# Optimization experiments

Measured on AMD Instinct MI355X. Metric: run time of the kernel, lower is better.

## Reference

```python
import jax, jax.numpy as jnp
from jax import lax
import numpy as np

# Mamba mixer dims (mamba-1.4b scale)
D_MODEL, D_INNER, D_STATE, D_CONV, DT_RANK = 2048, 4096, 16, 4, 128
B, L = 2, 1024


def setup_inputs() -> dict:
    key = jax.random.key(0)
    ks = jax.random.split(key, 10)
    s = 0.02
    x = jax.random.normal(ks[0], (B, L, D_MODEL), jnp.float32)
    W_in = jax.random.normal(ks[1], (2 * D_INNER, D_MODEL), jnp.float32) * s
    conv_w = jax.random.normal(ks[2], (D_INNER, D_CONV), jnp.float32) * s  # depthwise kernel
    conv_b = jax.random.normal(ks[3], (D_INNER,), jnp.float32) * s
    W_x = jax.random.normal(ks[4], (DT_RANK + 2 * D_STATE, D_INNER), jnp.float32) * s
    W_dt = jax.random.normal(ks[5], (D_INNER, DT_RANK), jnp.float32) * s
    b_dt = jax.random.normal(ks[6], (D_INNER,), jnp.float32) * s
    # S4D-real init: A = -[1..d_state] per channel
    A_log = jnp.log(jnp.broadcast_to(jnp.arange(1, D_STATE + 1, dtype=jnp.float32), (D_INNER, D_STATE)))
    Dp = jnp.ones((D_INNER,), jnp.float32)
    W_out = jax.random.normal(ks[7], (D_MODEL, D_INNER), jnp.float32) * s
    return {"x": x, "W_in": W_in, "conv_w": conv_w, "conv_b": conv_b,
            "W_x": W_x, "W_dt": W_dt, "b_dt": b_dt, "A_log": A_log,
            "Dp": Dp, "W_out": W_out}


def reference(x, W_in, conv_w, conv_b, W_x, W_dt, b_dt, A_log, Dp, W_out):
    b, l, _ = x.shape
    d_inner, d_state = A_log.shape
    dt_rank = W_dt.shape[1]
    d_conv = conv_w.shape[1]

    # in_proj -> x branch and gate z   [b,l,2*d_inner]
    xz = jnp.einsum('bld,ed->ble', x, W_in)
    xp, z = jnp.split(xz, 2, axis=-1)

    # causal depthwise conv1d (kernel size d_conv) + SiLU
    xpad = jnp.pad(xp, ((0, 0), (d_conv - 1, 0), (0, 0)))
    xc = conv_b + sum(xpad[:, k:k + l, :] * conv_w[:, k] for k in range(d_conv))
    xc = jax.nn.silu(xc)

    # input-dependent dt, B, C
    dbc = jnp.einsum('ble,fe->blf', xc, W_x)
    dt = dbc[..., :dt_rank]
    Bm = dbc[..., dt_rank:dt_rank + d_state]          # [b,l,s]
    Cm = dbc[..., dt_rank + d_state:]                 # [b,l,s]
    delta = jax.nn.softplus(jnp.einsum('blr,er->ble', dt, W_dt) + b_dt)  # [b,l,e]

    A = -jnp.exp(A_log)                               # [e,s]
    dA = jnp.exp(delta[..., None] * A)                # [b,l,e,s]
    dBx = delta[..., None] * Bm[:, :, None, :] * xc[..., None]  # [b,l,e,s]

    def step(h, inp):
        dA_t, dBx_t = inp                             # [b,e,s]
        h = dA_t * h + dBx_t
        return h, h

    h0 = jnp.zeros((b, d_inner, d_state), x.dtype)
    _, hs = lax.scan(step, h0, (jnp.swapaxes(dA, 0, 1), jnp.swapaxes(dBx, 0, 1)))
    hs = jnp.swapaxes(hs, 0, 1)                       # [b,l,e,s]

    y = jnp.einsum('bles,bls->ble', hs, Cm) + xc * Dp
    y = y * jax.nn.silu(z)
    return jnp.einsum('ble,de->bld', y, W_out)
```

## Files before the change

### kernel.cpp

```cpp
#include <hip/hip_runtime.h>
#include <cstdint>


typedef __bf16 bf16x8 __attribute__((ext_vector_type(8)));
typedef float f32x4 __attribute__((ext_vector_type(4)));

__device__ __forceinline__ unsigned short f2bf(float f) {
  uint32_t u = __float_as_uint(f);
  u += 0x7FFFu + ((u >> 16) & 1u);
  return (unsigned short)(u >> 16);
}

__device__ __forceinline__ float silu_f(float v) {
  return v / (1.f + __expf(-v));
}

__device__ __forceinline__ float softplus_f(float v) {
  return (v > 20.f) ? v : log1pf(__expf(v));
}

__global__ void cast_f32_to_bf16(const float* __restrict__ src,
                                 unsigned short* __restrict__ dst, int n4) {
  int i = blockIdx.x * 256 + threadIdx.x;
  if (i >= n4) return;
  float4 v = reinterpret_cast<const float4*>(src)[i];
  ushort4 o;
  o.x = f2bf(v.x); o.y = f2bf(v.y); o.z = f2bf(v.z); o.w = f2bf(v.w);
  reinterpret_cast<ushort4*>(dst)[i] = o;
}

__global__ void cast_wx_pad(const float* __restrict__ Wx,
                            unsigned short* __restrict__ dst) {
  int i = blockIdx.x * 256 + threadIdx.x;
  int r = i >> 12;
  float v = (r < 160) ? Wx[(size_t)r * 4096 + (i & 4095)] : 0.f;
  dst[i] = f2bf(v);
}

#define BM 128
#define BN 128
#define BKK 32

__device__ __forceinline__ void stage_tile(const unsigned short* __restrict__ G,
                                           int ldK, int g0, int k0,
                                           unsigned short* lds, int wave, int lane) {
#pragma unroll
  for (int c = 0; c < 2; ++c) {
    int row = c * 64 + wave * 16 + (lane >> 2);
    int col = (lane & 3) * 8;
    const unsigned short* src = G + (size_t)(g0 + row) * ldK + (k0 + col);
    unsigned short* dst = lds + c * 2048 + wave * 512;
    __builtin_amdgcn_global_load_lds((__attribute__((address_space(1))) void*)(src),
                                     (__attribute__((address_space(3))) void*)(dst),
                                     16, 0, 0);
  }
}

__global__ __launch_bounds__(256)
void gemm_bt(const unsigned short* __restrict__ A, const unsigned short* __restrict__ B,
             float* __restrict__ C, int M, int N, int ldK, int kchunk,
             const float* __restrict__ bias_sp) {
  __shared__ unsigned short As[BM * BKK];
  __shared__ unsigned short Bs[BN * BKK];
  const int tid = threadIdx.x;
  const int wave = tid >> 6, lane = tid & 63;
  const int wr = wave >> 1, wc = wave & 1;
  const int m0 = blockIdx.y * BM, n0 = blockIdx.x * BN;
  const int lr = lane & 15, lg = lane >> 4;
  const int kb = blockIdx.z * kchunk, ke = kb + kchunk;
  C += (size_t)blockIdx.z * M * N;

  f32x4 zero = {0.f, 0.f, 0.f, 0.f};
  f32x4 acc[4][4];
#pragma unroll
  for (int i = 0; i < 4; ++i)
#pragma unroll
    for (int j = 0; j < 4; ++j) acc[i][j] = zero;

  for (int k0 = kb; k0 < ke; k0 += BKK) {
    stage_tile(A, ldK, m0, k0, As, wave, lane);
    stage_tile(B, ldK, n0, k0, Bs, wave, lane);
    __syncthreads();
    bf16x8 af[4], bfr[4];
#pragma unroll
    for (int i = 0; i < 4; ++i)
      af[i] = *reinterpret_cast<const bf16x8*>(&As[(wr * 64 + i * 16 + lr) * BKK + lg * 8]);
#pragma unroll
    for (int j = 0; j < 4; ++j)
      bfr[j] = *reinterpret_cast<const bf16x8*>(&Bs[(wc * 64 + j * 16 + lr) * BKK + lg * 8]);
#pragma unroll
    for (int i = 0; i < 4; ++i)
#pragma unroll
      for (int j = 0; j < 4; ++j)
        acc[i][j] = __builtin_amdgcn_mfma_f32_16x16x32_bf16(af[i], bfr[j], acc[i][j], 0, 0, 0);
    __syncthreads();
  }

#pragma unroll
  for (int i = 0; i < 4; ++i) {
#pragma unroll
    for (int j = 0; j < 4; ++j) {
      int mrow = m0 + wr * 64 + i * 16 + lg * 4;
      int ncol = n0 + wc * 64 + j * 16 + lr;
      if (bias_sp) {
        float bv = bias_sp[ncol];
#pragma unroll
        for (int r = 0; r < 4; ++r)
          C[(size_t)(mrow + r) * N + ncol] = softplus_f(acc[i][j][r] + bv);
      } else {
#pragma unroll
        for (int r = 0; r < 4; ++r)
          C[(size_t)(mrow + r) * N + ncol] = acc[i][j][r];
      }
    }
  }
}

__global__ void reduce8_dbc(const float* __restrict__ p, float* __restrict__ dbc,
                            unsigned short* __restrict__ dt_bf) {
  int i = blockIdx.x * 256 + threadIdx.x;
  float s = 0.f;
#pragma unroll
  for (int c = 0; c < 8; ++c) s += p[(size_t)c * 524288 + i];
  dbc[i] = s;
  int col = i & 255;
  if (col < 128) dt_bf[(size_t)(i >> 8) * 128 + col] = f2bf(s);
}

__global__ void reduce2_out(const float* __restrict__ p, float* __restrict__ out) {
  int i = blockIdx.x * 256 + threadIdx.x;
  const float4* p4 = reinterpret_cast<const float4*>(p);
  float4 a = p4[i], b = p4[i + 1048576];
  float4 r; r.x = a.x + b.x; r.y = a.y + b.y; r.z = a.z + b.z; r.w = a.w + b.w;
  reinterpret_cast<float4*>(out)[i] = r;
}

__global__ __launch_bounds__(512, 2)
void gemm_bt_8ph(const unsigned short* __restrict__ A,
                 const unsigned short* __restrict__ B,
                 float* __restrict__ C, int M, int N, int K, int nbm) {
  __shared__ unsigned short As[2][16384];
  __shared__ unsigned short Bs[2][16384];
  const int tid = threadIdx.x;
  const int wid = tid >> 6, lane = tid & 63;
  const int wr = wid >> 2, wc = wid & 3;
  const int lr = lane & 15, lg = lane >> 4;

  const int cpx = gridDim.x >> 3;
  const int x = blockIdx.x;
  const int wg = (x & 7) * cpx + (x >> 3);
  const int bm = wg % nbm, bn = wg / nbm;
  const int m0 = bm * 256, n0 = bn * 256;

  const int strow = tid >> 3;
  const int stcol0 = (tid & 7) * 8;

  f32x4 acc[8][4];
  f32x4 zero = {0.f, 0.f, 0.f, 0.f};
#pragma unroll
  for (int i = 0; i < 8; ++i)
#pragma unroll
    for (int j = 0; j < 4; ++j) acc[i][j] = zero;

  const int nt = K / 64;

  auto QUANT = [&](int t, int q) {
    const int buf = t & 1;
    const unsigned short* G = (q < 2) ? A : B;
    const int g0 = ((q < 2) ? m0 : n0) + ((q & 1) ? 128 : 0);
    unsigned short* lds = ((q < 2) ? &As[buf][0] : &Bs[buf][0]) + ((q & 1) ? 8192 : 0);
    const int k0 = t * 64;
#pragma unroll
    for (int r = 0; r < 2; ++r) {
      int row = r * 64 + strow;
      int scol = stcol0 ^ ((row & 7) << 3);
      const unsigned short* src = G + (size_t)(g0 + row) * K + (k0 + scol);
      __builtin_amdgcn_global_load_lds(
          (__attribute__((address_space(1))) const void*)(src),
          (__attribute__((address_space(3))) void*)(lds + r * 4096 + tid * 8),
          16, 0, 0);
    }
  };

  auto RD_A = [&](int buf, int mf, int ks) -> bf16x8 {
    int row = wr * 128 + mf * 16 + lr;
    int col = (ks * 32 + lg * 8) ^ ((row & 7) << 3);
    return *reinterpret_cast<const bf16x8*>(&As[buf][row * 64 + col]);
  };
  auto RD_B = [&](int buf, int nf, int ks) -> bf16x8 {
    int row = wc * 64 + nf * 16 + lr;
    int col = (ks * 32 + lg * 8) ^ ((row & 7) << 3);
    return *reinterpret_cast<const bf16x8*>(&Bs[buf][row * 64 + col]);
  };

  QUANT(0, 0); QUANT(0, 1); QUANT(0, 2); QUANT(0, 3);
  QUANT(1, 0);

  bf16x8 a[4][2], b[4][2];
  for (int t = 0; t < nt; ++t) {
    const int buf = t & 1;
    const bool pf1 = (t + 1 < nt);
    if (pf1) {
      QUANT(t + 1, 1);
      asm volatile("s_waitcnt vmcnt(4)" ::: "memory");
    } else {
      asm volatile("s_waitcnt vmcnt(0)" ::: "memory");
    }
    __builtin_amdgcn_s_barrier();
#pragma unroll
    for (int mf = 0; mf < 4; ++mf)
#pragma unroll
      for (int ks = 0; ks < 2; ++ks) a[mf][ks] = RD_A(buf, mf, ks);
#pragma unroll
    for (int nf = 0; nf < 2; ++nf)
#pragma unroll
      for (int ks = 0; ks < 2; ++ks) b[nf][ks] = RD_B(buf, nf, ks);
    asm volatile("s_waitcnt lgkmcnt(0)" ::: "memory");
    __builtin_amdgcn_sched_barrier(0);
    __builtin_amdgcn_s_setprio(1);
#pragma unroll
    for (int nf = 0; nf < 2; ++nf)
#pragma unroll
      for (int mf = 0; mf < 4; ++mf)
#pragma unroll
        for (int ks = 0; ks < 2; ++ks)
          acc[mf][nf] = __builtin_amdgcn_mfma_f32_16x16x32_bf16(a[mf][ks], b[nf][ks], acc[mf][nf], 0, 0, 0);
    __builtin_amdgcn_s_setprio(0);
    if (pf1) QUANT(t + 1, 2);
#pragma unroll
    for (int nf = 2; nf < 4; ++nf)
#pragma unroll
      for (int ks = 0; ks < 2; ++ks) b[nf][ks] = RD_B(buf, nf, ks);
    asm volatile("s_waitcnt lgkmcnt(0)" ::: "memory");
    __builtin_amdgcn_sched_barrier(0);
    __builtin_amdgcn_s_setprio(1);
#pragma unroll
    for (int nf = 2; nf < 4; ++nf)
#pragma unroll
      for (int mf = 0; mf < 4; ++mf)
#pragma unroll
        for (int ks = 0; ks < 2; ++ks)
          acc[mf][nf] = __builtin_amdgcn_mfma_f32_16x16x32_bf16(a[mf][ks], b[nf][ks], acc[mf][nf], 0, 0, 0);
    __builtin_amdgcn_s_setprio(0);
    if (pf1) QUANT(t + 1, 3);
#pragma unroll
    for (int mf = 0; mf < 4; ++mf)
#pragma unroll
      for (int ks = 0; ks < 2; ++ks) a[mf][ks] = RD_A(buf, mf + 4, ks);
    asm volatile("s_waitcnt lgkmcnt(0)" ::: "memory");
    __builtin_amdgcn_sched_barrier(0);
    __builtin_amdgcn_s_setprio(1);
#pragma unroll
    for (int nf = 0; nf < 2; ++nf)
#pragma unroll
      for (int mf = 0; mf < 4; ++mf)
#pragma unroll
        for (int ks = 0; ks < 2; ++ks)
          acc[mf + 4][nf] = __builtin_amdgcn_mfma_f32_16x16x32_bf16(a[mf][ks], b[nf][ks], acc[mf + 4][nf], 0, 0, 0);
    __builtin_amdgcn_s_setprio(0);
    __builtin_amdgcn_s_barrier();
    if (t + 2 < nt) QUANT(t + 2, 0);
    __builtin_amdgcn_s_setprio(1);
#pragma unroll
    for (int nf = 2; nf < 4; ++nf)
#pragma unroll
      for (int mf = 0; mf < 4; ++mf)
#pragma unroll
        for (int ks = 0; ks < 2; ++ks)
          acc[mf + 4][nf] = __builtin_amdgcn_mfma_f32_16x16x32_bf16(a[mf][ks], b[nf][ks], acc[mf + 4][nf], 0, 0, 0);
    __builtin_amdgcn_s_setprio(0);
  }

#pragma unroll
  for (int mf = 0; mf < 8; ++mf) {
#pragma unroll
    for (int nf = 0; nf < 4; ++nf) {
      int mrow = m0 + wr * 128 + mf * 16 + lg * 4;
      int ncol = n0 + wc * 64 + nf * 16 + lr;
#pragma unroll
      for (int r = 0; r < 4; ++r)
        C[(size_t)(mrow + r) * N + ncol] = acc[mf][nf][r];
    }
  }
}

__global__ void conv_silu_kernel(const float* __restrict__ xz,
                                 const float* __restrict__ conv_w,
                                 const float* __restrict__ conv_b,
                                 float* __restrict__ xc,
                                 unsigned short* __restrict__ xc_bf) {
  int idx = blockIdx.x * 256 + threadIdx.x;
  int e = idx & 4095;
  int m = idx >> 12;
  int l = m & 1023;
  float acc = conv_b[e];
#pragma unroll
  for (int k = 0; k < 4; ++k) {
    int ls = l - 3 + k;
    if (ls >= 0) acc = fmaf(xz[(size_t)(m - 3 + k) * 8192 + e], conv_w[e * 4 + k], acc);
  }
  float s = silu_f(acc);
  xc[idx] = s;
  xc_bf[idx] = f2bf(s);
}

__global__ __launch_bounds__(256)
void scan_pass1(const float* __restrict__ delta, const float* __restrict__ dbc,
                const float* __restrict__ xc, const float* __restrict__ A_log,
                float* __restrict__ hfin, float* __restrict__ Pprod) {
  __shared__ float Bsh[1024];
  const int tid = threadIdx.x;
  const int bc = blockIdx.x >> 4;
  const int eg = blockIdx.x & 15;
  const int b = bc >> 4, c = bc & 15;
  const int e = eg * 256 + tid;
  const int mb = b * 1024 + c * 64;
  for (int i = tid; i < 1024; i += 256)
    Bsh[i] = dbc[(size_t)(mb + (i >> 4)) * 256 + 128 + (i & 15)];
  __syncthreads();

  float A[16];
  const float4* al = reinterpret_cast<const float4*>(A_log + (size_t)e * 16);
#pragma unroll
  for (int q = 0; q < 4; ++q) {
    float4 v = al[q];
    A[q * 4 + 0] = -__expf(v.x); A[q * 4 + 1] = -__expf(v.y);
    A[q * 4 + 2] = -__expf(v.z); A[q * 4 + 3] = -__expf(v.w);
  }
  float h[16], P[16];
#pragma unroll
  for (int s = 0; s < 16; ++s) { h[s] = 0.f; P[s] = 1.f; }

  for (int ll = 0; ll < 64; ++ll) {
    const size_t m = (size_t)(mb + ll);
    float dl = delta[m * 4096 + e];
    float dxc = dl * xc[m * 4096 + e];
#pragma unroll
    for (int s = 0; s < 16; ++s) {
      float dA = __expf(dl * A[s]);
      P[s] *= dA;
      h[s] = fmaf(dA, h[s], Bsh[ll * 16 + s] * dxc);
    }
  }
  float* hp = hfin + ((size_t)bc * 4096 + e) * 16;
  float* pp = Pprod + ((size_t)bc * 4096 + e) * 16;
#pragma unroll
  for (int s = 0; s < 16; ++s) { hp[s] = h[s]; pp[s] = P[s]; }
}

__global__ void scan_pass2(float* __restrict__ hfin, const float* __restrict__ Pprod) {
  int idx = blockIdx.x * 256 + threadIdx.x;
  int b = idx >> 16;
  int es = idx & 65535;
  float H = 0.f;
  for (int c = 0; c < 16; ++c) {
    size_t o = ((size_t)(b * 16 + c) << 16) + es;
    float hf = hfin[o];
    float Pp = Pprod[o];
    hfin[o] = H;
    H = fmaf(Pp, H, hf);
  }
}

__global__ __launch_bounds__(256)
void scan_pass3(const float* __restrict__ delta, const float* __restrict__ dbc,
                const float* __restrict__ xc, const float* __restrict__ xz,
                const float* __restrict__ A_log, const float* __restrict__ Dp,
                const float* __restrict__ hcarry, unsigned short* __restrict__ y_bf) {
  __shared__ float Bsh[1024];
  __shared__ float Csh[1024];
  const int tid = threadIdx.x;
  const int bc = blockIdx.x >> 4;
  const int eg = blockIdx.x & 15;
  const int b = bc >> 4, c = bc & 15;
  const int e = eg * 256 + tid;
  const int mb = b * 1024 + c * 64;
  for (int i = tid; i < 1024; i += 256) {
    size_t base = (size_t)(mb + (i >> 4)) * 256 + (i & 15);
    Bsh[i] = dbc[base + 128];
    Csh[i] = dbc[base + 144];
  }
  __syncthreads();

  float A[16];
  const float4* al = reinterpret_cast<const float4*>(A_log + (size_t)e * 16);
#pragma unroll
  for (int q = 0; q < 4; ++q) {
    float4 v = al[q];
    A[q * 4 + 0] = -__expf(v.x); A[q * 4 + 1] = -__expf(v.y);
    A[q * 4 + 2] = -__expf(v.z); A[q * 4 + 3] = -__expf(v.w);
  }
  float h[16];
  const float* hp = hcarry + ((size_t)bc * 4096 + e) * 16;
#pragma unroll
  for (int s = 0; s < 16; ++s) h[s] = hp[s];
  const float Dv = Dp[e];

  for (int ll = 0; ll < 64; ++ll) {
    const size_t m = (size_t)(mb + ll);
    float dl = delta[m * 4096 + e];
    float xcv = xc[m * 4096 + e];
    float dxc = dl * xcv;
    float y = 0.f;
#pragma unroll
    for (int s = 0; s < 16; ++s) {
      float dA = __expf(dl * A[s]);
      h[s] = fmaf(dA, h[s], Bsh[ll * 16 + s] * dxc);
      y = fmaf(h[s], Csh[ll * 16 + s], y);
    }
    float z = xz[m * 8192 + 4096 + e];
    y = (y + xcv * Dv) * silu_f(z);
    y_bf[m * 4096 + e] = f2bf(y);
  }
}

extern "C" void kernel_launch(void* const* d_in, const int* in_sizes, int n_in,
                              void* d_out, int out_size, void* d_ws, size_t ws_size,
                              hipStream_t stream) {
  const float* x      = (const float*)d_in[0];
  const float* W_in   = (const float*)d_in[1];
  const float* conv_w = (const float*)d_in[2];
  const float* conv_b = (const float*)d_in[3];
  const float* W_x    = (const float*)d_in[4];
  const float* W_dt   = (const float*)d_in[5];
  const float* b_dt   = (const float*)d_in[6];
  const float* A_log  = (const float*)d_in[7];
  const float* Dp     = (const float*)d_in[8];
  const float* W_out  = (const float*)d_in[9];
  float* out = (float*)d_out;
  char* ws = (char*)d_ws;

  unsigned short* Win_bf    = (unsigned short*)(ws + 0);
  float*          gpart     = (float*)(ws + 0);
  float*          delta     = (float*)(ws + 0);
  unsigned short* x_bf      = (unsigned short*)(ws + 33554432);
  unsigned short* y_bf      = (unsigned short*)(ws + 33554432);
  unsigned short* Wout_bf   = (unsigned short*)(ws + 50331648);
  unsigned short* Wx_bf     = (unsigned short*)(ws + 67108864);
  unsigned short* Wdt_bf    = (unsigned short*)(ws + 69206016);
  float*          xz        = (float*)(ws + 70254592);
  float*          xc        = (float*)(ws + 137363456);
  unsigned short* xc_bf     = (unsigned short*)(ws + 170917888);
  float*          hfin      = (float*)(ws + 170917888);
  float*          Pprod     = (float*)(ws + 179306496);
  float*          dbc       = (float*)(ws + 187695104);
  unsigned short* dt_bf     = (unsigned short*)(ws + 189792256);

  cast_f32_to_bf16<<<4096, 256, 0, stream>>>(x, x_bf, 1048576);
  cast_f32_to_bf16<<<16384, 256, 0, stream>>>(W_in, Win_bf, 4194304);
  cast_f32_to_bf16<<<8192, 256, 0, stream>>>(W_out, Wout_bf, 2097152);
  cast_wx_pad<<<4096, 256, 0, stream>>>(W_x, Wx_bf);
  cast_f32_to_bf16<<<512, 256, 0, stream>>>(W_dt, Wdt_bf, 131072);

  gemm_bt_8ph<<<256, 512, 0, stream>>>(x_bf, Win_bf, xz, 2048, 8192, 2048, 8);

  conv_silu_kernel<<<32768, 256, 0, stream>>>(xz, conv_w, conv_b, xc, xc_bf);

  gemm_bt<<<dim3(2, 16, 8), 256, 0, stream>>>(xc_bf, Wx_bf, gpart, 2048, 256, 4096, 512, nullptr);
  reduce8_dbc<<<2048, 256, 0, stream>>>(gpart, dbc, dt_bf);

  gemm_bt<<<dim3(32, 16, 1), 256, 0, stream>>>(dt_bf, Wdt_bf, delta, 2048, 4096, 128, 128, b_dt);

  scan_pass1<<<512, 256, 0, stream>>>(delta, dbc, xc, A_log, hfin, Pprod);
  scan_pass2<<<512, 256, 0, stream>>>(hfin, Pprod);
  scan_pass3<<<512, 256, 0, stream>>>(delta, dbc, xc, xz, A_log, Dp, hfin, y_bf);

  gemm_bt<<<dim3(16, 16, 2), 256, 0, stream>>>(y_bf, Wout_bf, gpart, 2048, 2048, 4096, 2048, nullptr);
  reduce2_out<<<4096, 256, 0, stream>>>(gpart, out);
}
```

Before: 384.7 us.

## Restructure in_proj GEMM LDS layout into k-halves and vectorize conv+SiLU

The in_proj GEMM now stores each 64-wide k-tile as two 32-wide halves with a new XOR swizzle. The main loop is reorganized so that all 8 A fragments for one k-half are loaded at once, with prefetch of the next tile's quarters interleaved between MFMA phases and extra barriers. This aims to reduce register pressure and improve overlap of global-to-LDS loads with compute, at the cost of more barriers per iteration. Separately, the depthwise conv+SiLU kernel processes four channels per thread using float4 loads and stores to cut instruction count and improve memory coalescing.

```diff
diff --git a/kernel.cpp b/kernel.cpp
--- a/kernel.cpp
+++ b/kernel.cpp
@@ -152,9 +152,6 @@
   const int bm = wg % nbm, bn = wg / nbm;
   const int m0 = bm * 256, n0 = bn * 256;
 
-  const int strow = tid >> 3;
-  const int stcol0 = (tid & 7) * 8;
-
   f32x4 acc[8][4];
   f32x4 zero = {0.f, 0.f, 0.f, 0.f};
 #pragma unroll
@@ -166,14 +163,15 @@
 
   auto QUANT = [&](int t, int q) {
     const int buf = t & 1;
-    const unsigned short* G = (q < 2) ? A : B;
-    const int g0 = ((q < 2) ? m0 : n0) + ((q & 1) ? 128 : 0);
-    unsigned short* lds = ((q < 2) ? &As[buf][0] : &Bs[buf][0]) + ((q & 1) ? 8192 : 0);
-    const int k0 = t * 64;
+    const int ks = q >> 1;
+    const unsigned short* G = (q & 1) ? B : A;
+    const int g0 = (q & 1) ? n0 : m0;
+    unsigned short* lds = ((q & 1) ? &Bs[buf][0] : &As[buf][0]) + ks * 8192;
+    const int k0 = t * 64 + ks * 32;
 #pragma unroll
     for (int r = 0; r < 2; ++r) {
-      int row = r * 64 + strow;
-      int scol = stcol0 ^ ((row & 7) << 3);
+      int row = r * 128 + (tid >> 2);
+      int scol = ((tid & 3) * 8) ^ (((row >> 1) & 3) << 3);
       const unsigned short* src = G + (size_t)(g0 + row) * K + (k0 + scol);
       __builtin_amdgcn_global_load_lds(
           (__attribute__((address_space(1))) const void*)(src),
@@ -182,93 +180,94 @@
     }
   };
 
-  auto RD_A = [&](int buf, int mf, int ks) -> bf16x8 {
+  auto RD_A = [&](int buf, int ks, int mf) -> bf16x8 {
     int row = wr * 128 + mf * 16 + lr;
-    int col = (ks * 32 + lg * 8) ^ ((row & 7) << 3);
-    return *reinterpret_cast<const bf16x8*>(&As[buf][row * 64 + col]);
+    int col = (lg * 8) ^ (((row >> 1) & 3) << 3);
+    return *reinterpret_cast<const bf16x8*>(&As[buf][ks * 8192 + row * 32 + col]);
   };
-  auto RD_B = [&](int buf, int nf, int ks) -> bf16x8 {
+  auto RD_B = [&](int buf, int ks, int nf) -> bf16x8 {
     int row = wc * 64 + nf * 16 + lr;
-    int col = (ks * 32 + lg * 8) ^ ((row & 7) << 3);
-    return *reinterpret_cast<const bf16x8*>(&Bs[buf][row * 64 + col]);
+    int col = (lg * 8) ^ (((row >> 1) & 3) << 3);
+    return *reinterpret_cast<const bf16x8*>(&Bs[buf][ks * 8192 + row * 32 + col]);
   };
 
   QUANT(0, 0); QUANT(0, 1); QUANT(0, 2); QUANT(0, 3);
-  QUANT(1, 0);
-
-  bf16x8 a[4][2], b[4][2];
+  asm volatile("s_waitcnt vmcnt(4)" ::: "memory");
+  __builtin_amdgcn_s_barrier();
+
+  bf16x8 a[8], b[4];
   for (int t = 0; t < nt; ++t) {
     const int buf = t & 1;
-    const bool pf1 = (t + 1 < nt);
-    if (pf1) {
+    const bool pf = (t + 1 < nt);
+#pragma unroll
+    for (int mf = 0; mf < 8; ++mf) a[mf] = RD_A(buf, 0, mf);
+    b[0] = RD_B(buf, 0, 0); b[1] = RD_B(buf, 0, 1);
+    if (pf) {
+      QUANT(t + 1, 0);
+      asm volatile("s_waitcnt vmcnt(6)" ::: "memory");
+    } else {
+      asm volatile("s_waitcnt vmcnt(4)" ::: "memory");
+    }
+    __builtin_amdgcn_s_barrier();
+    asm volatile("s_waitcnt lgkmcnt(0)" ::: "memory");
+    __builtin_amdgcn_sched_barrier(0);
+    __builtin_amdgcn_s_setprio(1);
+#pragma unroll
+    for (int nf = 0; nf < 2; ++nf)
+#pragma unroll
+      for (int mf = 0; mf < 8; ++mf)
+        acc[mf][nf] = __builtin_amdgcn_mfma_f32_16x16x32_bf16(a[mf], b[nf], acc[mf][nf], 0, 0, 0);
+    __builtin_amdgcn_s_setprio(0);
+    __builtin_amdgcn_s_barrier();
+    b[2] = RD_B(buf, 0, 2); b[3] = RD_B(buf, 0, 3);
+    if (pf) {
       QUANT(t + 1, 1);
       asm volatile("s_waitcnt vmcnt(4)" ::: "memory");
     } else {
       asm volatile("s_waitcnt vmcnt(0)" ::: "memory");
     }
     __builtin_amdgcn_s_barrier();
-#pragma unroll
-    for (int mf = 0; mf < 4; ++mf)
-#pragma unroll
-      for (int ks = 0; ks < 2; ++ks) a[mf][ks] = RD_A(buf, mf, ks);
-#pragma unroll
-    for (int nf = 0; nf < 2; ++nf)
-#pragma unroll
-      for (int ks = 0; ks < 2; ++ks) b[nf][ks] = RD_B(buf, nf, ks);
     asm volatile("s_waitcnt lgkmcnt(0)" ::: "memory");
     __builtin_amdgcn_sched_barrier(0);
     __builtin_amdgcn_s_setprio(1);
 #pragma unroll
-    for (int nf = 0; nf < 2; ++nf)
-#pragma unroll
-      for (int mf = 0; mf < 4; ++mf)
-#pragma unroll
-        for (int ks = 0; ks < 2; ++ks)
-          acc[mf][nf] = __builtin_amdgcn_mfma_f32_16x16x32_bf16(a[mf][ks], b[nf][ks], acc[mf][nf], 0, 0, 0);
+    for (int nf = 2; nf < 4; ++nf)
+#pragma unroll
+      for (int mf = 0; mf < 8; ++mf)
+        acc[mf][nf] = __builtin_amdgcn_mfma_f32_16x16x32_bf16(a[mf], b[nf], acc[mf][nf], 0, 0, 0);
     __builtin_amdgcn_s_setprio(0);
-    if (pf1) QUANT(t + 1, 2);
-#pragma unroll
-    for (int nf = 2; nf < 4; ++nf)
-#pragma unroll
-      for (int ks = 0; ks < 2; ++ks) b[nf][ks] = RD_B(buf, nf, ks);
+    __builtin_amdgcn_s_barrier();
+#pragma unroll
+    for (int mf = 0; mf < 8; ++mf) a[mf] = RD_A(buf, 1, mf);
+    b[0] = RD_B(buf, 1, 0); b[1] = RD_B(buf, 1, 1);
+    if (pf) QUANT(t + 1, 2);
+    __builtin_amdgcn_s_barrier();
     asm volatile("s_waitcnt lgkmcnt(0)" ::: "memory");
     __builtin_amdgcn_sched_barrier(0);
     __builtin_amdgcn_s_setprio(1);
 #pragma unroll
-    for (int nf = 2; nf < 4; ++nf)
-#pragma unroll
-      for (int mf = 0; mf < 4; ++mf)
-#pragma unroll
-        for (int ks = 0; ks < 2; ++ks)
-          acc[mf][nf] = __builtin_amdgcn_mfma_f32_16x16x32_bf16(a[mf][ks], b[nf][ks], acc[mf][nf], 0, 0, 0);
+    for (int nf = 0; nf < 2; ++nf)
+#pragma unroll
+      for (int mf = 0; mf < 8; ++mf)
+        acc[mf][nf] = __builtin_amdgcn_mfma_f32_16x16x32_bf16(a[mf], b[nf], acc[mf][nf], 0, 0, 0);
     __builtin_amdgcn_s_setprio(0);
-    if (pf1) QUANT(t + 1, 3);
-#pragma unroll
-    for (int mf = 0; mf < 4; ++mf)
-#pragma unroll
-      for (int ks = 0; ks < 2; ++ks) a[mf][ks] = RD_A(buf, mf + 4, ks);
+    __builtin_amdgcn_s_barrier();
+    b[2] = RD_B(buf, 1, 2); b[3] = RD_B(buf, 1, 3);
+    if (pf) {
+      QUANT(t + 1, 3);
+      asm volatile("s_waitcnt vmcnt(4)" ::: "memory");
+    }
+    __builtin_amdgcn_s_barrier();
     asm volatile("s_waitcnt lgkmcnt(0)" ::: "memory");
     __builtin_amdgcn_sched_barrier(0);
     __builtin_amdgcn_s_setprio(1);
 #pragma unroll
-    for (int nf = 0; nf < 2; ++nf)
-#pragma unroll
-      for (int mf = 0; mf < 4; ++mf)
-#pragma unroll
-        for (int ks = 0; ks < 2; ++ks)
-          acc[mf + 4][nf] = __builtin_amdgcn_mfma_f32_16x16x32_bf16(a[mf][ks], b[nf][ks], acc[mf + 4][nf], 0, 0, 0);
+    for (int nf = 2; nf < 4; ++nf)
+#pragma unroll
+      for (int mf = 0; mf < 8; ++mf)
+        acc[mf][nf] = __builtin_amdgcn_mfma_f32_16x16x32_bf16(a[mf], b[nf], acc[mf][nf], 0, 0, 0);
     __builtin_amdgcn_s_setprio(0);
     __builtin_amdgcn_s_barrier();
-    if (t + 2 < nt) QUANT(t + 2, 0);
-    __builtin_amdgcn_s_setprio(1);
-#pragma unroll
-    for (int nf = 2; nf < 4; ++nf)
-#pragma unroll
-      for (int mf = 0; mf < 4; ++mf)
-#pragma unroll
-        for (int ks = 0; ks < 2; ++ks)
-          acc[mf + 4][nf] = __builtin_amdgcn_mfma_f32_16x16x32_bf16(a[mf][ks], b[nf][ks], acc[mf + 4][nf], 0, 0, 0);
-    __builtin_amdgcn_s_setprio(0);
   }
 
 #pragma unroll
@@ -289,19 +288,32 @@
                                  const float* __restrict__ conv_b,
                                  float* __restrict__ xc,
                                  unsigned short* __restrict__ xc_bf) {
-  int idx = blockIdx.x * 256 + threadIdx.x;
-  int e = idx & 4095;
-  int m = idx >> 12;
+  int i4 = blockIdx.x * 256 + threadIdx.x;
+  int e4 = i4 & 1023;
+  int m = i4 >> 10;
   int l = m & 1023;
-  float acc = conv_b[e];
+  float4 cw0 = reinterpret_cast<const float4*>(conv_w)[e4 * 4 + 0];
+  float4 cw1 = reinterpret_cast<const float4*>(conv_w)[e4 * 4 + 1];
+  float4 cw2 = reinterpret_cast<const float4*>(conv_w)[e4 * 4 + 2];
+  float4 cw3 = reinterpret_cast<const float4*>(conv_w)[e4 * 4 + 3];
+  float4 acc = reinterpret_cast<const float4*>(conv_b)[e4];
 #pragma unroll
   for (int k = 0; k < 4; ++k) {
-    int ls = l - 3 + k;
-    if (ls >= 0) acc = fmaf(xz[(size_t)(m - 3 + k) * 8192 + e], conv_w[e * 4 + k], acc);
-  }
-  float s = silu_f(acc);
-  xc[idx] = s;
-  xc_bf[idx] = f2bf(s);
+    if (l - 3 + k >= 0) {
+      float4 xv = reinterpret_cast<const float4*>(xz)[(size_t)(m - 3 + k) * 2048 + e4];
+      acc.x = fmaf(xv.x, ((const float*)&cw0)[k], acc.x);
+      acc.y = fmaf(xv.y, ((const float*)&cw1)[k], acc.y);
+      acc.z = fmaf(xv.z, ((const float*)&cw2)[k], acc.z);
+      acc.w = fmaf(xv.w, ((const float*)&cw3)[k], acc.w);
+    }
+  }
+  float4 s;
+  s.x = silu_f(acc.x); s.y = silu_f(acc.y);
+  s.z = silu_f(acc.z); s.w = silu_f(acc.w);
+  reinterpret_cast<float4*>(xc)[i4] = s;
+  ushort4 o;
+  o.x = f2bf(s.x); o.y = f2bf(s.y); o.z = f2bf(s.z); o.w = f2bf(s.w);
+  reinterpret_cast<ushort4*>(xc_bf)[i4] = o;
 }
 
 __global__ __launch_bounds__(256)
@@ -454,7 +466,7 @@
 
   gemm_bt_8ph<<<256, 512, 0, stream>>>(x_bf, Win_bf, xz, 2048, 8192, 2048, 8);
 
-  conv_silu_kernel<<<32768, 256, 0, stream>>>(xz, conv_w, conv_b, xc, xc_bf);
+  conv_silu_kernel<<<8192, 256, 0, stream>>>(xz, conv_w, conv_b, xc, xc_bf);
 
   gemm_bt<<<dim3(2, 16, 8), 256, 0, stream>>>(xc_bf, Wx_bf, gpart, 2048, 256, 4096, 512, nullptr);
   reduce8_dbc<<<2048, 256, 0, stream>>>(gpart, dbc, dt_bf);
```

After: 366.6 us. 1.05x faster.
